# Performance work log

Measured on AMD Instinct MI355X. Metric: run time of the kernel, lower is better.

## Reference

```python
import jax, jax.numpy as jnp
import numpy as np

N_NODES = 50000
N_EDGES = 800000
IN_CH = 128
HID = 64
OUT_CH = 10
N_LAYERS = 5
N_GRAPHS = 128
BN_EPS = 1e-5


def setup_inputs() -> dict:
    key = jax.random.key(0)
    ks = jax.random.split(key, 20)
    s = 0.1
    inp = {}
    inp["x"] = jax.random.normal(ks[0], (N_NODES, IN_CH), jnp.float32)
    inp["edge_index"] = jax.random.randint(ks[1], (2, N_EDGES), 0, N_NODES, dtype=jnp.int32)
    inp["batch"] = jnp.sort(jax.random.randint(ks[2], (N_NODES,), 0, N_GRAPHS, dtype=jnp.int32))
    # GINConv MLPs: layer 0 maps IN_CH->HID->HID, layers 1..4 map HID->HID->HID
    inp["w1_0"] = jax.random.normal(ks[3], (IN_CH, HID), jnp.float32) * s
    inp["b1_0"] = jnp.zeros((HID,), jnp.float32)
    inp["w2_0"] = jax.random.normal(ks[4], (HID, HID), jnp.float32) * s
    inp["b2_0"] = jnp.zeros((HID,), jnp.float32)
    inp["w1_rest"] = jax.random.normal(ks[5], (N_LAYERS - 1, HID, HID), jnp.float32) * s
    inp["b1_rest"] = jnp.zeros((N_LAYERS - 1, HID), jnp.float32)
    inp["w2_rest"] = jax.random.normal(ks[6], (N_LAYERS - 1, HID, HID), jnp.float32) * s
    inp["b2_rest"] = jnp.zeros((N_LAYERS - 1, HID), jnp.float32)
    # JK 'cat' projection: Linear(N_LAYERS*HID -> HID)
    inp["jk_w"] = jax.random.normal(ks[7], (N_LAYERS * HID, HID), jnp.float32) * s
    inp["jk_b"] = jnp.zeros((HID,), jnp.float32)
    # classifier MLP([HID, HID, OUT]) with batch_norm between
    inp["clf_w1"] = jax.random.normal(ks[8], (HID, HID), jnp.float32) * s
    inp["clf_b1"] = jnp.zeros((HID,), jnp.float32)
    inp["bn_gamma"] = jnp.ones((HID,), jnp.float32)
    inp["bn_beta"] = jnp.zeros((HID,), jnp.float32)
    inp["clf_w2"] = jax.random.normal(ks[9], (HID, OUT_CH), jnp.float32) * s
    inp["clf_b2"] = jnp.zeros((OUT_CH,), jnp.float32)
    return inp


def reference(x, edge_index, batch, w1_0, b1_0, w2_0, b2_0,
              w1_rest, b1_rest, w2_rest, b2_rest, jk_w, jk_b,
              clf_w1, clf_b1, bn_gamma, bn_beta, clf_w2, clf_b2):
    src, dst = edge_index[0], edge_index[1]
    xs = []
    h = x
    for i in range(N_LAYERS):
        # GINConv: mlp((1+eps)*x + sum_{j in N(i)} x_j), eps=0
        agg = jax.ops.segment_sum(h[src], dst, num_segments=N_NODES)  # [N, d]
        z = agg + h
        if i == 0:
            w1, b1, w2, b2 = w1_0, b1_0, w2_0, b2_0
        else:
            w1, b1, w2, b2 = w1_rest[i - 1], b1_rest[i - 1], w2_rest[i - 1], b2_rest[i - 1]
        h = jax.nn.relu(z @ w1 + b1) @ w2 + b2
        # BasicGNN post-conv activation (dropout disabled in inference)
        h = jax.nn.relu(h)
        xs.append(h)
    # JumpingKnowledge 'cat' + projection back to HID
    h = jnp.concatenate(xs, axis=-1) @ jk_w + jk_b  # [N, HID]
    # global_add_pool: per-graph sum
    g = jax.ops.segment_sum(h, batch, num_segments=N_GRAPHS)  # [G, HID]
    # classifier MLP with batch_norm (batch statistics)
    t = g @ clf_w1 + clf_b1
    mu = t.mean(axis=0)
    var = ((t - mu) ** 2).mean(axis=0)
    t = (t - mu) * jax.lax.rsqrt(var + BN_EPS) * bn_gamma + bn_beta
    t = jax.nn.relu(t)
    return t @ clf_w2 + clf_b2  # [G, OUT]
```

## Files before the change

kernel.cpp:

```cpp
#include <hip/hip_runtime.h>
#include <hip/hip_fp16.h>

#define NN 50000
#define NE 800000
#define NG 128
#define OUTC 10
#define SCAN_NB ((NN + 255) / 256)
#define NTILE 3125

__global__ void count_kernel(const int* __restrict__ dst, int* __restrict__ cnt) {
  for (int e = blockIdx.x * blockDim.x + threadIdx.x; e < NE; e += gridDim.x * blockDim.x)
    atomicAdd(&cnt[dst[e]], 1);
}

__global__ __launch_bounds__(256) void partial_kernel(const int* __restrict__ cnt,
                                                      int* __restrict__ part) {
  __shared__ int red[256];
  const int t = threadIdx.x;
  const int idx = blockIdx.x * 256 + t;
  red[t] = (idx < NN) ? cnt[idx] : 0;
  __syncthreads();
#pragma unroll
  for (int off = 128; off > 0; off >>= 1) {
    if (t < off) red[t] += red[t + off];
    __syncthreads();
  }
  if (t == 0) part[blockIdx.x] = red[0];
}

__global__ __launch_bounds__(256) void scanpart_kernel(int* __restrict__ part) {
  __shared__ int s[256];
  const int t = threadIdx.x;
  s[t] = (t < SCAN_NB) ? part[t] : 0;
  __syncthreads();
#pragma unroll
  for (int off = 1; off < 256; off <<= 1) {
    const int v = (t >= off) ? s[t - off] : 0;
    __syncthreads();
    s[t] += v;
    __syncthreads();
  }
  if (t < SCAN_NB) part[t] = (t == 0) ? 0 : s[t - 1];
}

__global__ __launch_bounds__(256) void scatter_scan_kernel(const int* __restrict__ cnt,
                                                           const int* __restrict__ part,
                                                           int* __restrict__ rowptr,
                                                           int* __restrict__ cursor) {
  __shared__ int s[256];
  const int t = threadIdx.x;
  const int idx = blockIdx.x * 256 + t;
  s[t] = (idx < NN) ? cnt[idx] : 0;
  __syncthreads();
#pragma unroll
  for (int off = 1; off < 256; off <<= 1) {
    const int v = (t >= off) ? s[t - off] : 0;
    __syncthreads();
    s[t] += v;
    __syncthreads();
  }
  const int excl = part[blockIdx.x] + ((t == 0) ? 0 : s[t - 1]);
  if (idx < NN) { rowptr[idx] = excl; cursor[idx] = excl; }
  if (idx == 0) rowptr[NN] = NE;
}

__global__ void fill_kernel(const int* __restrict__ src, const int* __restrict__ dst,
                            int* __restrict__ cursor, int* __restrict__ esrc) {
  for (int e = blockIdx.x * blockDim.x + threadIdx.x; e < NE; e += gridDim.x * blockDim.x) {
    int p = atomicAdd(&cursor[dst[e]], 1);
    esrc[p] = src[e];
  }
}

__global__ __launch_bounds__(128) void gbounds_kernel(const int* __restrict__ batch,
                                                      float* __restrict__ gcnt) {
  __shared__ int sb[NG + 1];
  const int g = threadIdx.x;
  int lo = 0, hi = NN;
  while (lo < hi) {
    const int mid = (lo + hi) >> 1;
    if (batch[mid] < g) lo = mid + 1; else hi = mid;
  }
  sb[g] = lo;
  if (g == 0) sb[NG] = NN;
  __syncthreads();
  gcnt[g] = (float)(sb[g + 1] - sb[g]);
}

__global__ __launch_bounds__(256) void proj_kernel(const float* __restrict__ x,
                                                   const float* __restrict__ w1,
                                                   __half* __restrict__ y) {
  __shared__ float sW[128 * 64];
  __shared__ float sX[64 * 128];
  const int t = threadIdx.x, c = t & 63, rg = t >> 6;
  for (int i = t; i < 128 * 64; i += 256) sW[i] = w1[i];
  const int ntiles = (NN + 63) / 64;
  for (int tile = blockIdx.x; tile < ntiles; tile += gridDim.x) {
    const int r0 = tile * 64, nv = min(64, NN - r0);
    __syncthreads();
    for (int i = t; i < nv * 32; i += 256)
      ((float4*)sX)[i] = ((const float4*)(x + (size_t)r0 * 128))[i];
    __syncthreads();
    float acc[16];
#pragma unroll
    for (int i = 0; i < 16; ++i) acc[i] = 0.f;
    for (int k = 0; k < 128; k += 4) {
      const float w0 = sW[(k + 0) * 64 + c], w1v = sW[(k + 1) * 64 + c],
                  w2v = sW[(k + 2) * 64 + c], w3v = sW[(k + 3) * 64 + c];
#pragma unroll
      for (int i = 0; i < 16; ++i) {
        const float4 xv = *(const float4*)&sX[(rg * 16 + i) * 128 + k];
        acc[i] = fmaf(xv.x, w0, acc[i]);
        acc[i] = fmaf(xv.y, w1v, acc[i]);
        acc[i] = fmaf(xv.z, w2v, acc[i]);
        acc[i] = fmaf(xv.w, w3v, acc[i]);
      }
    }
#pragma unroll
    for (int i = 0; i < 16; ++i) {
      const int r = rg * 16 + i;
      if (r < nv) y[(size_t)(r0 + r) * 64 + c] = __float2half(acc[i]);
    }
  }
}

__global__ __launch_bounds__(256, 8) void agg_kernel(const __half* __restrict__ h,
                                                     const int* __restrict__ rowptr,
                                                     const int* __restrict__ esrc,
                                                     float* __restrict__ z) {
  const int ln = threadIdx.x & 63, wv = threadIdx.x >> 6;
  const int oct = ln >> 3, i = ln & 7;
  const int row = blockIdx.x * 4 + wv;
  if (row >= NN) return;
  const int beg = rowptr[row], end = rowptr[row + 1];
  union H8 { float4 f; __half2 h2[4]; };
  float acc[8];
  if (oct == 0) {
    H8 u; u.f = *(const float4*)(h + (size_t)row * 64 + i * 8);
#pragma unroll
    for (int k = 0; k < 4; ++k) {
      const float2 f = __half22float2(u.h2[k]);
      acc[2 * k] = f.x; acc[2 * k + 1] = f.y;
    }
  } else {
#pragma unroll
    for (int k = 0; k < 8; ++k) acc[k] = 0.f;
  }
  int e = beg + oct;
  for (; e + 8 < end; e += 16) {
    const int s0 = esrc[e], s1 = esrc[e + 8];
    H8 u0, u1;
    u0.f = *(const float4*)(h + (size_t)s0 * 64 + i * 8);
    u1.f = *(const float4*)(h + (size_t)s1 * 64 + i * 8);
#pragma unroll
    for (int k = 0; k < 4; ++k) {
      const float2 f0 = __half22float2(u0.h2[k]);
      const float2 f1 = __half22float2(u1.h2[k]);
      acc[2 * k]     += f0.x + f1.x;
      acc[2 * k + 1] += f0.y + f1.y;
    }
  }
  for (; e < end; e += 8) {
    const int s0 = esrc[e];
    H8 u0;
    u0.f = *(const float4*)(h + (size_t)s0 * 64 + i * 8);
#pragma unroll
    for (int k = 0; k < 4; ++k) {
      const float2 f0 = __half22float2(u0.h2[k]);
      acc[2 * k] += f0.x; acc[2 * k + 1] += f0.y;
    }
  }
#pragma unroll
  for (int off = 8; off < 64; off <<= 1) {
#pragma unroll
    for (int k = 0; k < 8; ++k) acc[k] += __shfl_xor(acc[k], off);
  }
  if (oct == 0) {
    const float4 lo = {acc[0], acc[1], acc[2], acc[3]};
    const float4 hi = {acc[4], acc[5], acc[6], acc[7]};
    *(float4*)(z + (size_t)row * 64 + i * 8) = lo;
    *(float4*)(z + (size_t)row * 64 + i * 8 + 4) = hi;
  }
}

template <bool HASW1, bool WRITEH>
__global__ __launch_bounds__(256) void mlp_kernel(
    const float* __restrict__ z, const float* __restrict__ w1,
    const float* __restrict__ b1, const float* __restrict__ w2,
    const float* __restrict__ b2, __half* __restrict__ hout,
    const int* __restrict__ batch, float* __restrict__ gl) {
  __shared__ float sS[4][16 * 64];
  const int t = threadIdx.x, c = t & 63, wv = t >> 6;
  const int wg = blockIdx.x * 4 + wv;
  if (wg >= NTILE) return;
  float* slice = &sS[wv][0];
  const int n0 = wg * 16;
  const float b1c = b1[c], b2c = b2[c];

  float zr[16];
#pragma unroll
  for (int r = 0; r < 16; ++r) zr[r] = z[(size_t)(n0 + r) * 64 + c];
  if (!HASW1) {
#pragma unroll
    for (int r = 0; r < 16; ++r) zr[r] = fmaxf(zr[r] + b1c, 0.f);
  }
#pragma unroll
  for (int r = 0; r < 16; ++r) slice[r * 64 + c] = zr[r];

  if (HASW1) {
    float acc[16];
#pragma unroll
    for (int r = 0; r < 16; ++r) acc[r] = b1c;
    for (int kc = 0; kc < 4; ++kc) {
      float wr[16];
#pragma unroll
      for (int j = 0; j < 16; ++j) wr[j] = w1[(kc * 16 + j) * 64 + c];
#pragma unroll
      for (int r = 0; r < 16; ++r) {
        const float* zp = &slice[r * 64 + kc * 16];
        const float4 za = *(const float4*)(zp + 0);
        const float4 zb = *(const float4*)(zp + 4);
        const float4 zc = *(const float4*)(zp + 8);
        const float4 zd = *(const float4*)(zp + 12);
        float a = acc[r];
        a = fmaf(za.x, wr[0], a);  a = fmaf(za.y, wr[1], a);
        a = fmaf(za.z, wr[2], a);  a = fmaf(za.w, wr[3], a);
        a = fmaf(zb.x, wr[4], a);  a = fmaf(zb.y, wr[5], a);
        a = fmaf(zb.z, wr[6], a);  a = fmaf(zb.w, wr[7], a);
        a = fmaf(zc.x, wr[8], a);  a = fmaf(zc.y, wr[9], a);
        a = fmaf(zc.z, wr[10], a); a = fmaf(zc.w, wr[11], a);
        a = fmaf(zd.x, wr[12], a); a = fmaf(zd.y, wr[13], a);
        a = fmaf(zd.z, wr[14], a); a = fmaf(zd.w, wr[15], a);
        acc[r] = a;
      }
    }
#pragma unroll
    for (int r = 0; r < 16; ++r) slice[r * 64 + c] = fmaxf(acc[r], 0.f);
  }

  float acc2[16];
#pragma unroll
  for (int r = 0; r < 16; ++r) acc2[r] = b2c;
  for (int kc = 0; kc < 4; ++kc) {
    float wr[16];
#pragma unroll
    for (int j = 0; j < 16; ++j) wr[j] = w2[(kc * 16 + j) * 64 + c];
#pragma unroll
    for (int r = 0; r < 16; ++r) {
      const float* hp = &slice[r * 64 + kc * 16];
      const float4 za = *(const float4*)(hp + 0);
      const float4 zb = *(const float4*)(hp + 4);
      const float4 zc = *(const float4*)(hp + 8);
      const float4 zd = *(const float4*)(hp + 12);
      float a = acc2[r];
      a = fmaf(za.x, wr[0], a);  a = fmaf(za.y, wr[1], a);
      a = fmaf(za.z, wr[2], a);  a = fmaf(za.w, wr[3], a);
      a = fmaf(zb.x, wr[4], a);  a = fmaf(zb.y, wr[5], a);
      a = fmaf(zb.z, wr[6], a);  a = fmaf(zb.w, wr[7], a);
      a = fmaf(zc.x, wr[8], a);  a = fmaf(zc.y, wr[9], a);
      a = fmaf(zc.z, wr[10], a); a = fmaf(zc.w, wr[11], a);
      a = fmaf(zd.x, wr[12], a); a = fmaf(zd.y, wr[13], a);
      a = fmaf(zd.z, wr[14], a); a = fmaf(zd.w, wr[15], a);
      acc2[r] = a;
    }
  }
  float pacc = 0.f;
  int cur = batch[n0];
#pragma unroll
  for (int r = 0; r < 16; ++r) {
    const float hval = fmaxf(acc2[r], 0.f);
    if (WRITEH) hout[(size_t)(n0 + r) * 64 + c] = __float2half(hval);
    const int b = batch[n0 + r];
    if (b != cur) {
      atomicAdd(&gl[(size_t)cur * 64 + c], pacc);
      pacc = 0.f;
      cur = b;
    }
    pacc += hval;
  }
  atomicAdd(&gl[(size_t)cur * 64 + c], pacc);
}

__global__ __launch_bounds__(64) void jk_fold_kernel(
    const float* __restrict__ g5, const float* __restrict__ gcnt,
    const float* __restrict__ jkw, const float* __restrict__ jkb,
    const float* __restrict__ w1, const float* __restrict__ b1,
    float* __restrict__ tmat) {
  __shared__ float sg[64];
  const int gi = blockIdx.x, c = threadIdx.x;
  float a = jkb[c] * gcnt[gi];
  for (int l = 0; l < 5; ++l) {
    const float* gv = &g5[(size_t)(l * NG + gi) * 64];
    const float* wv = &jkw[(size_t)l * 64 * 64];
#pragma unroll 8
    for (int k = 0; k < 64; ++k) a = fmaf(gv[k], wv[k * 64 + c], a);
  }
  sg[c] = a;
  __syncthreads();
  float tv = b1[c];
#pragma unroll 8
  for (int k = 0; k < 64; ++k) tv = fmaf(sg[k], w1[k * 64 + c], tv);
  tmat[gi * 64 + c] = tv;
}

__global__ __launch_bounds__(256) void bn_out_kernel(
    const float* __restrict__ tmat, const float* __restrict__ gamma,
    const float* __restrict__ beta, const float* __restrict__ w2,
    const float* __restrict__ b2, float* __restrict__ out) {
  __shared__ float sT[NG * 64];
  __shared__ float sW2[64 * OUTC];
  __shared__ float sMu[64], sRs[64];
  const int t = threadIdx.x;
  for (int i = t; i < NG * 64; i += 256) sT[i] = tmat[i];
  for (int i = t; i < 64 * OUTC; i += 256) sW2[i] = w2[i];
  __syncthreads();
  if (t < 64) {
    float s = 0.f;
    for (int gi = 0; gi < NG; ++gi) s += sT[gi * 64 + t];
    const float mu = s / NG;
    float v = 0.f;
    for (int gi = 0; gi < NG; ++gi) { const float d = sT[gi * 64 + t] - mu; v += d * d; }
    v /= NG;
    sMu[t] = mu;
    sRs[t] = rsqrtf(v + 1e-5f);
  }
  __syncthreads();
  for (int idx = t; idx < NG * 64; idx += 256) {
    const int cc = idx & 63;
    sT[idx] = fmaxf((sT[idx] - sMu[cc]) * sRs[cc] * gamma[cc] + beta[cc], 0.f);
  }
  __syncthreads();
  for (int idx = t; idx < NG * OUTC; idx += 256) {
    const int gi = idx / OUTC, o = idx % OUTC;
    float a = b2[o];
    for (int k = 0; k < 64; ++k) a = fmaf(sT[gi * 64 + k], sW2[k * OUTC + o], a);
    out[idx] = a;
  }
}

extern "C" void kernel_launch(void* const* d_in, const int* in_sizes, int n_in,
                              void* d_out, int out_size, void* d_ws, size_t ws_size,
                              hipStream_t stream) {
  const float* x     = (const float*)d_in[0];
  const int*   ei    = (const int*)d_in[1];
  const int*   batch = (const int*)d_in[2];
  const float* w1_0  = (const float*)d_in[3];
  const float* b1_0  = (const float*)d_in[4];
  const float* w2_0  = (const float*)d_in[5];
  const float* b2_0  = (const float*)d_in[6];
  const float* w1_r  = (const float*)d_in[7];
  const float* b1_r  = (const float*)d_in[8];
  const float* w2_r  = (const float*)d_in[9];
  const float* b2_r  = (const float*)d_in[10];
  const float* jk_w  = (const float*)d_in[11];
  const float* jk_b  = (const float*)d_in[12];
  const float* cw1   = (const float*)d_in[13];
  const float* cb1   = (const float*)d_in[14];
  const float* bng   = (const float*)d_in[15];
  const float* bnb   = (const float*)d_in[16];
  const float* cw2   = (const float*)d_in[17];
  const float* cb2   = (const float*)d_in[18];
  float* out = (float*)d_out;

  char* base = (char*)d_ws;
  size_t o = 0;
  auto take = [&](size_t n) { char* p = base + o; o = (o + n + 255) & ~(size_t)255; return p; };
  int*    cnt    = (int*)take((size_t)NN * 4);
  int*    rowptr = (int*)take((size_t)(NN + 1) * 4);
  int*    cursor = (int*)take((size_t)NN * 4);
  int*    part   = (int*)take((size_t)SCAN_NB * 4);
  int*    esrc   = (int*)take((size_t)NE * 4);
  __half* hA     = (__half*)take((size_t)NN * 64 * 2);
  __half* hB     = (__half*)take((size_t)NN * 64 * 2);
  float*  z      = (float*)take((size_t)NN * 64 * 4);
  float*  g5     = (float*)take((size_t)5 * NG * 64 * 4);
  float*  gcnt   = (float*)take((size_t)NG * 4);
  float*  tmat   = (float*)take((size_t)NG * 64 * 4);
  (void)ws_size; (void)in_sizes; (void)n_in; (void)out_size;

  hipMemsetAsync(cnt, 0, (size_t)NN * 4, stream);
  hipMemsetAsync(g5, 0, (size_t)5 * NG * 64 * 4, stream);

  const int* src = ei;
  const int* dst = ei + NE;
  count_kernel<<<1024, 256, 0, stream>>>(dst, cnt);
  partial_kernel<<<SCAN_NB, 256, 0, stream>>>(cnt, part);
  scanpart_kernel<<<1, 256, 0, stream>>>(part);
  scatter_scan_kernel<<<SCAN_NB, 256, 0, stream>>>(cnt, part, rowptr, cursor);
  fill_kernel<<<1024, 256, 0, stream>>>(src, dst, cursor, esrc);
  gbounds_kernel<<<1, 128, 0, stream>>>(batch, gcnt);

  const int MLP_GRID = (NTILE + 3) / 4;

  proj_kernel<<<512, 256, 0, stream>>>(x, w1_0, hB);
  agg_kernel<<<(NN + 3) / 4, 256, 0, stream>>>(hB, rowptr, esrc, z);
  mlp_kernel<false, true><<<MLP_GRID, 256, 0, stream>>>(z, nullptr, b1_0, w2_0, b2_0,
                                                        hA, batch, g5);
  const __half* hin = hA;
  __half* hout = hB;
  for (int l = 1; l < 5; ++l) {
    agg_kernel<<<(NN + 3) / 4, 256, 0, stream>>>(hin, rowptr, esrc, z);
    if (l < 4) {
      mlp_kernel<true, true><<<MLP_GRID, 256, 0, stream>>>(
          z, w1_r + (size_t)(l - 1) * 64 * 64, b1_r + (size_t)(l - 1) * 64,
          w2_r + (size_t)(l - 1) * 64 * 64, b2_r + (size_t)(l - 1) * 64, hout,
          batch, g5 + (size_t)l * NG * 64);
    } else {
      mlp_kernel<true, false><<<MLP_GRID, 256, 0, stream>>>(
          z, w1_r + (size_t)(l - 1) * 64 * 64, b1_r + (size_t)(l - 1) * 64,
          w2_r + (size_t)(l - 1) * 64 * 64, b2_r + (size_t)(l - 1) * 64, hout,
          batch, g5 + (size_t)l * NG * 64);
    }
    __half* tmp = (__half*)hin;
    hin = hout;
    hout = tmp;
  }

  jk_fold_kernel<<<NG, 64, 0, stream>>>(g5, gcnt, jk_w, jk_b, cw1, cb1, tmat);
  bn_out_kernel<<<1, 256, 0, stream>>>(tmat, bng, bnb, cw2, cb2, out);
}
```

Measured before the change: 450.8 us.

## Fuse neighbor aggregation into the GIN MLP kernel and drop the z buffer

Fuses the CSR gather-sum aggregation into the per-layer MLP kernel. Each group of 8 lanes aggregates two rows straight into shared memory, so the fp32 z intermediate is never written to or read from global memory and one launch per layer goes away. In exchange, parallelism during the gather drops from one wave per row to 8 lanes per row processed serially. Load imbalance across rows of different degree now stalls the whole MLP tile.

```diff
diff --git a/kernel.cpp b/kernel.cpp
--- a/kernel.cpp
+++ b/kernel.cpp
@@ -124,89 +124,107 @@
   }
 }
 
-__global__ __launch_bounds__(256, 8) void agg_kernel(const __half* __restrict__ h,
-                                                     const int* __restrict__ rowptr,
-                                                     const int* __restrict__ esrc,
-                                                     float* __restrict__ z) {
-  const int ln = threadIdx.x & 63, wv = threadIdx.x >> 6;
-  const int oct = ln >> 3, i = ln & 7;
-  const int row = blockIdx.x * 4 + wv;
-  if (row >= NN) return;
-  const int beg = rowptr[row], end = rowptr[row + 1];
-  union H8 { float4 f; __half2 h2[4]; };
-  float acc[8];
-  if (oct == 0) {
-    H8 u; u.f = *(const float4*)(h + (size_t)row * 64 + i * 8);
-#pragma unroll
-    for (int k = 0; k < 4; ++k) {
-      const float2 f = __half22float2(u.h2[k]);
-      acc[2 * k] = f.x; acc[2 * k + 1] = f.y;
-    }
-  } else {
-#pragma unroll
-    for (int k = 0; k < 8; ++k) acc[k] = 0.f;
-  }
-  int e = beg + oct;
-  for (; e + 8 < end; e += 16) {
-    const int s0 = esrc[e], s1 = esrc[e + 8];
-    H8 u0, u1;
-    u0.f = *(const float4*)(h + (size_t)s0 * 64 + i * 8);
-    u1.f = *(const float4*)(h + (size_t)s1 * 64 + i * 8);
-#pragma unroll
-    for (int k = 0; k < 4; ++k) {
-      const float2 f0 = __half22float2(u0.h2[k]);
-      const float2 f1 = __half22float2(u1.h2[k]);
-      acc[2 * k]     += f0.x + f1.x;
-      acc[2 * k + 1] += f0.y + f1.y;
-    }
-  }
-  for (; e < end; e += 8) {
-    const int s0 = esrc[e];
-    H8 u0;
-    u0.f = *(const float4*)(h + (size_t)s0 * 64 + i * 8);
-#pragma unroll
-    for (int k = 0; k < 4; ++k) {
-      const float2 f0 = __half22float2(u0.h2[k]);
-      acc[2 * k] += f0.x; acc[2 * k + 1] += f0.y;
-    }
-  }
-#pragma unroll
-  for (int off = 8; off < 64; off <<= 1) {
-#pragma unroll
-    for (int k = 0; k < 8; ++k) acc[k] += __shfl_xor(acc[k], off);
-  }
-  if (oct == 0) {
-    const float4 lo = {acc[0], acc[1], acc[2], acc[3]};
-    const float4 hi = {acc[4], acc[5], acc[6], acc[7]};
-    *(float4*)(z + (size_t)row * 64 + i * 8) = lo;
-    *(float4*)(z + (size_t)row * 64 + i * 8 + 4) = hi;
-  }
-}
-
 template <bool HASW1, bool WRITEH>
-__global__ __launch_bounds__(256) void mlp_kernel(
-    const float* __restrict__ z, const float* __restrict__ w1,
-    const float* __restrict__ b1, const float* __restrict__ w2,
-    const float* __restrict__ b2, __half* __restrict__ hout,
-    const int* __restrict__ batch, float* __restrict__ gl) {
+__global__ __launch_bounds__(256) void gin_fused_kernel(
+    const __half* __restrict__ hin, const int* __restrict__ rowptr,
+    const int* __restrict__ esrc,
+    const float* __restrict__ w1, const float* __restrict__ b1,
+    const float* __restrict__ w2, const float* __restrict__ b2,
+    __half* __restrict__ hout, const int* __restrict__ batch,
+    float* __restrict__ gl) {
   __shared__ float sS[4][16 * 64];
   const int t = threadIdx.x, c = t & 63, wv = t >> 6;
   const int wg = blockIdx.x * 4 + wv;
   if (wg >= NTILE) return;
   float* slice = &sS[wv][0];
   const int n0 = wg * 16;
+  const int oct = c >> 3, i = c & 7;
+
+  const int rA = n0 + 2 * oct;
+  const int pA0 = rowptr[rA], pA1 = rowptr[rA + 1], pB1 = rowptr[rA + 2];
+  union H8 { float4 f; __half2 h2[4]; };
+  const __half* hch = hin + i * 8;
+  float zA[8], zB[8];
+  {
+    H8 u0, u1;
+    u0.f = *(const float4*)(hch + (size_t)rA * 64);
+    u1.f = *(const float4*)(hch + (size_t)(rA + 1) * 64);
+#pragma unroll
+    for (int k = 0; k < 4; ++k) {
+      const float2 f0 = __half22float2(u0.h2[k]);
+      const float2 f1 = __half22float2(u1.h2[k]);
+      zA[2 * k] = f0.x; zA[2 * k + 1] = f0.y;
+      zB[2 * k] = f1.x; zB[2 * k + 1] = f1.y;
+    }
+  }
+  int e = pA0;
+  for (; e + 1 < pA1; e += 2) {
+    const int s0 = esrc[e], s1 = esrc[e + 1];
+    H8 u0, u1;
+    u0.f = *(const float4*)(hch + (size_t)s0 * 64);
+    u1.f = *(const float4*)(hch + (size_t)s1 * 64);
+#pragma unroll
+    for (int k = 0; k < 4; ++k) {
+      const float2 f0 = __half22float2(u0.h2[k]);
+      const float2 f1 = __half22float2(u1.h2[k]);
+      zA[2 * k]     += f0.x + f1.x;
+      zA[2 * k + 1] += f0.y + f1.y;
+    }
+  }
+  if (e < pA1) {
+    H8 u0; u0.f = *(const float4*)(hch + (size_t)esrc[e] * 64);
+#pragma unroll
+    for (int k = 0; k < 4; ++k) {
+      const float2 f0 = __half22float2(u0.h2[k]);
+      zA[2 * k] += f0.x; zA[2 * k + 1] += f0.y;
+    }
+  }
+  e = pA1;
+  for (; e + 1 < pB1; e += 2) {
+    const int s0 = esrc[e], s1 = esrc[e + 1];
+    H8 u0, u1;
+    u0.f = *(const float4*)(hch + (size_t)s0 * 64);
+    u1.f = *(const float4*)(hch + (size_t)s1 * 64);
+#pragma unroll
+    for (int k = 0; k < 4; ++k) {
+      const float2 f0 = __half22float2(u0.h2[k]);
+      const float2 f1 = __half22float2(u1.h2[k]);
+      zB[2 * k]     += f0.x + f1.x;
+      zB[2 * k + 1] += f0.y + f1.y;
+    }
+  }
+  if (e < pB1) {
+    H8 u0; u0.f = *(const float4*)(hch + (size_t)esrc[e] * 64);
+#pragma unroll
+    for (int k = 0; k < 4; ++k) {
+      const float2 f0 = __half22float2(u0.h2[k]);
+      zB[2 * k] += f0.x; zB[2 * k + 1] += f0.y;
+    }
+  }
+  if (!HASW1) {
+    const float4 blo = *(const float4*)(b1 + i * 8);
+    const float4 bhi = *(const float4*)(b1 + i * 8 + 4);
+    zA[0] = fmaxf(zA[0] + blo.x, 0.f); zA[1] = fmaxf(zA[1] + blo.y, 0.f);
+    zA[2] = fmaxf(zA[2] + blo.z, 0.f); zA[3] = fmaxf(zA[3] + blo.w, 0.f);
+    zA[4] = fmaxf(zA[4] + bhi.x, 0.f); zA[5] = fmaxf(zA[5] + bhi.y, 0.f);
+    zA[6] = fmaxf(zA[6] + bhi.z, 0.f); zA[7] = fmaxf(zA[7] + bhi.w, 0.f);
+    zB[0] = fmaxf(zB[0] + blo.x, 0.f); zB[1] = fmaxf(zB[1] + blo.y, 0.f);
+    zB[2] = fmaxf(zB[2] + blo.z, 0.f); zB[3] = fmaxf(zB[3] + blo.w, 0.f);
+    zB[4] = fmaxf(zB[4] + bhi.x, 0.f); zB[5] = fmaxf(zB[5] + bhi.y, 0.f);
+    zB[6] = fmaxf(zB[6] + bhi.z, 0.f); zB[7] = fmaxf(zB[7] + bhi.w, 0.f);
+  }
+  {
+    const float4 a0 = {zA[0], zA[1], zA[2], zA[3]};
+    const float4 a1 = {zA[4], zA[5], zA[6], zA[7]};
+    const float4 b0v = {zB[0], zB[1], zB[2], zB[3]};
+    const float4 b1v_ = {zB[4], zB[5], zB[6], zB[7]};
+    *(float4*)&slice[(2 * oct) * 64 + i * 8] = a0;
+    *(float4*)&slice[(2 * oct) * 64 + i * 8 + 4] = a1;
+    *(float4*)&slice[(2 * oct + 1) * 64 + i * 8] = b0v;
+    *(float4*)&slice[(2 * oct + 1) * 64 + i * 8 + 4] = b1v_;
+  }
+
   const float b1c = b1[c], b2c = b2[c];
-
-  float zr[16];
-#pragma unroll
-  for (int r = 0; r < 16; ++r) zr[r] = z[(size_t)(n0 + r) * 64 + c];
-  if (!HASW1) {
-#pragma unroll
-    for (int r = 0; r < 16; ++r) zr[r] = fmaxf(zr[r] + b1c, 0.f);
-  }
-#pragma unroll
-  for (int r = 0; r < 16; ++r) slice[r * 64 + c] = zr[r];
-
   if (HASW1) {
     float acc[16];
 #pragma unroll
@@ -372,7 +390,6 @@
   int*    esrc   = (int*)take((size_t)NE * 4);
   __half* hA     = (__half*)take((size_t)NN * 64 * 2);
   __half* hB     = (__half*)take((size_t)NN * 64 * 2);
-  float*  z      = (float*)take((size_t)NN * 64 * 4);
   float*  g5     = (float*)take((size_t)5 * NG * 64 * 4);
   float*  gcnt   = (float*)take((size_t)NG * 4);
   float*  tmat   = (float*)take((size_t)NG * 64 * 4);
@@ -390,26 +407,24 @@
   fill_kernel<<<1024, 256, 0, stream>>>(src, dst, cursor, esrc);
   gbounds_kernel<<<1, 128, 0, stream>>>(batch, gcnt);
 
-  const int MLP_GRID = (NTILE + 3) / 4;
+  const int GRID = (NTILE + 3) / 4;
 
   proj_kernel<<<512, 256, 0, stream>>>(x, w1_0, hB);
-  agg_kernel<<<(NN + 3) / 4, 256, 0, stream>>>(hB, rowptr, esrc, z);
-  mlp_kernel<false, true><<<MLP_GRID, 256, 0, stream>>>(z, nullptr, b1_0, w2_0, b2_0,
-                                                        hA, batch, g5);
+  gin_fused_kernel<false, true><<<GRID, 256, 0, stream>>>(
+      hB, rowptr, esrc, nullptr, b1_0, w2_0, b2_0, hA, batch, g5);
   const __half* hin = hA;
   __half* hout = hB;
   for (int l = 1; l < 5; ++l) {
-    agg_kernel<<<(NN + 3) / 4, 256, 0, stream>>>(hin, rowptr, esrc, z);
     if (l < 4) {
-      mlp_kernel<true, true><<<MLP_GRID, 256, 0, stream>>>(
-          z, w1_r + (size_t)(l - 1) * 64 * 64, b1_r + (size_t)(l - 1) * 64,
-          w2_r + (size_t)(l - 1) * 64 * 64, b2_r + (size_t)(l - 1) * 64, hout,
-          batch, g5 + (size_t)l * NG * 64);
+      gin_fused_kernel<true, true><<<GRID, 256, 0, stream>>>(
+          hin, rowptr, esrc, w1_r + (size_t)(l - 1) * 64 * 64,
+          b1_r + (size_t)(l - 1) * 64, w2_r + (size_t)(l - 1) * 64 * 64,
+          b2_r + (size_t)(l - 1) * 64, hout, batch, g5 + (size_t)l * NG * 64);
     } else {
-      mlp_kernel<true, false><<<MLP_GRID, 256, 0, stream>>>(
-          z, w1_r + (size_t)(l - 1) * 64 * 64, b1_r + (size_t)(l - 1) * 64,
-          w2_r + (size_t)(l - 1) * 64 * 64, b2_r + (size_t)(l - 1) * 64, hout,
-          batch, g5 + (size_t)l * NG * 64);
+      gin_fused_kernel<true, false><<<GRID, 256, 0, stream>>>(
+          hin, rowptr, esrc, w1_r + (size_t)(l - 1) * 64 * 64,
+          b1_r + (size_t)(l - 1) * 64, w2_r + (size_t)(l - 1) * 64 * 64,
+          b2_r + (size_t)(l - 1) * 64, hout, batch, g5 + (size_t)l * NG * 64);
     }
     __half* tmp = (__half*)hin;
     hin = hout;
```

Result: faster. 427.6 us (-5.1%).
